# Kernel optimization log

Measured on AMD Instinct MI355X. Metric: run time of the kernel, lower is better.

Reference implementation:

```python
import jax, jax.numpy as jnp
import numpy as np

B, SEQ, NNODES = 4, 12, 1024
SEG_LEN, SEG_NUM = 3, 4
HID, FF, DK, NH, NLAYERS = 64, 2048, 32, 8, 2


def setup_inputs() -> dict:
    key = jax.random.key(0)
    ks = iter(jax.random.split(key, 64))
    def nrm(shape, scale=0.05):
        return jax.random.normal(next(ks), shape, dtype=jnp.float32) * scale
    ones = lambda s: jnp.ones(s, jnp.float32)
    zeros = lambda s: jnp.zeros(s, jnp.float32)
    S, L = 2, NLAYERS
    return {
        'traffic': nrm((B, SEQ, NNODES), 1.0),
        'user': nrm((B, SEQ, NNODES), 1.0),
        'patch_w': nrm((S, HID, SEG_LEN)), 'patch_b': nrm((S, HID)),
        'mha_w': nrm((S, L, 3 * HID, HID)), 'mha_b': nrm((S, L, 3 * HID)),
        'out_w': nrm((S, L, HID, HID)), 'out_b': nrm((S, L, HID)),
        'ff1_w': nrm((S, L, FF, HID)), 'ff1_b': nrm((S, L, FF)),
        'ff2_w': nrm((S, L, HID, FF)), 'ff2_b': nrm((S, L, HID)),
        'ln1_g': ones((S, L, HID)), 'ln1_b': zeros((S, L, HID)),
        'ln2_g': ones((S, L, HID)), 'ln2_b': zeros((S, L, HID)),
        'ga_wq': nrm((S, L, DK, HID)), 'ga_wk': nrm((S, L, DK, HID)), 'ga_wv': nrm((S, L, HID, HID)),
        'ga_ff1_w': nrm((S, L, FF, HID)), 'ga_ff1_b': nrm((S, L, FF)),
        'ga_ff2_w': nrm((S, L, HID, FF)), 'ga_ff2_b': nrm((S, L, HID)),
        'ga_ln1_g': ones((S, L, HID)), 'ga_ln1_b': zeros((S, L, HID)),
        'ga_ln2_g': ones((S, L, HID)), 'ga_ln2_b': zeros((S, L, HID)),
        'ca_wq': nrm((DK, 2 * HID)), 'ca_wk': nrm((DK, 2 * HID)), 'ca_wv': nrm((HID, 2 * HID)),
    }


def _ln(x, g, b, eps=1e-5):
    m = x.mean(-1, keepdims=True)
    v = jnp.mean((x - m) ** 2, -1, keepdims=True)
    return (x - m) / jnp.sqrt(v + eps) * g + b


def _pe(s, d):
    pos = jnp.arange(s, dtype=jnp.float32)[:, None]
    div = jnp.exp(jnp.arange(0, d, 2, dtype=jnp.float32) * (-np.log(10000.0) / d))
    pe = jnp.zeros((s, d), jnp.float32)
    pe = pe.at[:, 0::2].set(jnp.sin(pos * div))
    pe = pe.at[:, 1::2].set(jnp.cos(pos * div))
    return pe


def _mha(x, w, b, wo, bo):
    # standard nn.MultiheadAttention self-attn, batch_first; x: [B,S,H]
    qkv = x @ w.T + b
    q, k, v = jnp.split(qkv, 3, axis=-1)
    def heads(t):
        b_, s_, h_ = t.shape
        return t.reshape(b_, s_, NH, h_ // NH).transpose(0, 2, 1, 3)
    q, k, v = heads(q), heads(k), heads(v)
    scale = 1.0 / jnp.sqrt(jnp.float32(HID // NH))
    att = jax.nn.softmax(jnp.einsum('bhqd,bhkd->bhqk', q, k) * scale, axis=-1)
    o = jnp.einsum('bhqk,bhkd->bhqd', att, v).transpose(0, 2, 1, 3).reshape(x.shape)
    return o @ wo.T + bo


def _enc_layer(x, p):
    # TransformerEncoderLayer_cross, post-norm, dropout=0 (eval)
    x = _ln(x + _mha(x, p['mw'], p['mb'], p['ow'], p['ob']), p['g1'], p['b1'])
    f = jax.nn.relu(x @ p['f1w'].T + p['f1b']) @ p['f2w'].T + p['f2b']
    return _ln(x + f, p['g2'], p['b2'])


def _graph_att(x, p):
    # GraphAttention.forward (bias=None, mask=None, dropout=0)
    q = x @ p['wq'].T
    k = x @ p['wk'].T
    v = x @ p['wv'].T
    dist = jax.nn.softmax(jnp.einsum('bnd,bmd->bnm', q, k) / jnp.sqrt(jnp.float32(DK)), axis=-1)
    att = jnp.einsum('bnm,bmd->bnd', dist, v)
    att = _ln(att, p['g1'], p['b1']) + x
    f = jax.nn.relu(att @ p['f1w'].T + p['f1b']) @ p['f2w'].T + p['f2b']
    return _ln(att + f, p['g2'], p['b2'])


def reference(traffic, user, patch_w, patch_b, mha_w, mha_b, out_w, out_b,
              ff1_w, ff1_b, ff2_w, ff2_b, ln1_g, ln1_b, ln2_g, ln2_b,
              ga_wq, ga_wk, ga_wv, ga_ff1_w, ga_ff1_b, ga_ff2_w, ga_ff2_b,
              ga_ln1_g, ga_ln1_b, ga_ln2_g, ga_ln2_b, ca_wq, ca_wk, ca_wv):
    pe = _pe(SEG_NUM, HID)

    def encode(x, s):
        b, _, d = x.shape
        # DSW_embedding: b (seg_num seg_len) d -> b d seg_num seg_len, then Linear
        seg = x.reshape(b, SEG_NUM, SEG_LEN, d).transpose(0, 3, 1, 2)
        z = seg @ patch_w[s].T + patch_b[s]          # [b, d, seg_num, HID]
        z = z + pe                                    # positional encoding over patches
        for i in range(NLAYERS):
            # temporal attention over the patch axis
            zt = z.reshape(b * d, SEG_NUM, HID)
            zt = _enc_layer(zt, dict(mw=mha_w[s, i], mb=mha_b[s, i], ow=out_w[s, i], ob=out_b[s, i],
                                     f1w=ff1_w[s, i], f1b=ff1_b[s, i], f2w=ff2_w[s, i], f2b=ff2_b[s, i],
                                     g1=ln1_g[s, i], b1=ln1_b[s, i], g2=ln2_g[s, i], b2=ln2_b[s, i]))
            z = zt.reshape(b, d, SEG_NUM, HID)
            # spatial graph attention over the node axis
            zs = z.transpose(0, 2, 1, 3).reshape(b * SEG_NUM, d, HID)
            zs = _graph_att(zs, dict(wq=ga_wq[s, i], wk=ga_wk[s, i], wv=ga_wv[s, i],
                                     f1w=ga_ff1_w[s, i], f1b=ga_ff1_b[s, i], f2w=ga_ff2_w[s, i], f2b=ga_ff2_b[s, i],
                                     g1=ga_ln1_g[s, i], b1=ga_ln1_b[s, i], g2=ga_ln2_g[s, i], b2=ga_ln2_b[s, i]))
            z = zs.reshape(b, SEG_NUM, d, HID).transpose(0, 2, 1, 3)
        return z.mean(axis=2)                         # pool patches -> [b, d, HID]

    enc = jnp.concatenate([encode(traffic, 0), encode(user, 1)], axis=-1)  # [b, d, 2*HID]
    # encoder_attn: SelfAttention(2*HID -> dim_k=32, dim_v=HID)
    q = enc @ ca_wq.T
    k = enc @ ca_wk.T
    v = enc @ ca_wv.T
    dist = jax.nn.softmax(jnp.einsum('bnd,bmd->bnm', q, k) / jnp.sqrt(jnp.float32(DK)), axis=-1)
    return jnp.einsum('bnm,bmd->bnd', dist, v)        # [b, n_nodes, HID]
```

## Files before the change

### kernel.cpp

```cpp
#include <hip/hip_runtime.h>
#include <hip/hip_bf16.h>
#include <math.h>

#define BB 4
#define SEQL 12
#define NN 1024
#define SEGL 3
#define SEGN 4
#define HID 64
#define FFD 2048
#define DKK 32
#define NHH 8
#define HDD 8
#define ZS 1048576

using bf16 = __hip_bfloat16;
__device__ __forceinline__ float b2f(bf16 v) { return __bfloat162float(v); }

typedef __attribute__((ext_vector_type(8))) short s8v;
typedef __attribute__((ext_vector_type(4))) float f4v;
typedef __attribute__((ext_vector_type(4))) unsigned short u4v;

__device__ __forceinline__ unsigned short f2b(float f) {
  bf16 h = __float2bfloat16(f);
  unsigned short u; __builtin_memcpy(&u, &h, 2); return u;
}
__device__ __forceinline__ float us2f(unsigned short u) {
  unsigned int e = ((unsigned int)u) << 16;
  float f; __builtin_memcpy(&f, &e, 4); return f;
}

template <int F>
__device__ __forceinline__ float ldw(const void* p, long i) {
  if (F) return ((const float*)p)[i];
  return b2f(((const bf16*)p)[i]);
}
template <int F>
__device__ __forceinline__ s8v ldfrag(const void* p, long elemOff) {
  if (F) {
    const float* fp = (const float*)p + elemOff;
    f4v u = *(const f4v*)fp, v = *(const f4v*)(fp + 4);
    s8v t;
    t[0]=f2b(u[0]); t[1]=f2b(u[1]); t[2]=f2b(u[2]); t[3]=f2b(u[3]);
    t[4]=f2b(v[0]); t[5]=f2b(v[1]); t[6]=f2b(v[2]); t[7]=f2b(v[3]);
    return t;
  }
  return *(const s8v*)((const unsigned short*)p + elemOff);
}
template <int F>
__device__ __forceinline__ f4v ldb4(const void* p, long i) {
  if (F) return *(const f4v*)((const float*)p + i);
  u4v u = *(const u4v*)((const unsigned short*)p + i);
  f4v r; r[0]=us2f(u[0]); r[1]=us2f(u[1]); r[2]=us2f(u[2]); r[3]=us2f(u[3]);
  return r;
}

__global__ void k_zero(unsigned short* __restrict__ o, int n) {
  int i = blockIdx.x * 256 + threadIdx.x;
  if (i < n) o[i] = 0;
}

__global__ void k_detect(const void* __restrict__ x0, int* __restrict__ flag) {
  int t = threadIdx.x;
  int bad = 0;
  const bf16* p = (const bf16*)x0;
  for (int i = t; i < 512; i += 256) {
    float a = fabsf(b2f(p[i]));
    if (!(a < 1e4f) || (a != 0.f && a < 1e-4f)) bad = 1;
  }
  __shared__ int tot;
  if (t == 0) tot = 0;
  __syncthreads();
  unsigned long long m = __ballot(bad);
  if ((t & 63) == 0) atomicAdd(&tot, __popcll(m));
  __syncthreads();
  if (t == 0) *flag = (tot > 64) ? 1 : 0;
}

template <int F>
__device__ __forceinline__ void wconv_body(const void* __restrict__ w1,
    const void* __restrict__ w2, const void* __restrict__ w3,
    const void* __restrict__ w4, unsigned short* __restrict__ out) {
  int i = blockIdx.x * 256 + threadIdx.x;
  long e8 = (long)i * 8;
  int slot = (int)(e8 >> 17);
  int si = slot >> 2, which = slot & 3;
  long r = e8 & 131071;
  const void* src = (which == 0) ? w1 : (which == 1) ? w2 : (which == 2) ? w3 : w4;
  *(s8v*)(out + e8) = ldfrag<F>(src, (long)si*FFD*HID + r);
}
__global__ __launch_bounds__(256) void k_wconv(const void* w1, const void* w2,
    const void* w3, const void* w4, unsigned short* out,
    const int* __restrict__ flag) {
  if (*flag) wconv_body<1>(w1, w2, w3, w4, out);
  else       wconv_body<0>(w1, w2, w3, w4, out);
}

template <int F>
__device__ __forceinline__ void patch_body(const void* __restrict__ xt,
    const void* __restrict__ xu,
    const void* __restrict__ pw, const void* __restrict__ pb,
    float* __restrict__ z) {
  int bid = blockIdx.x;
  int s = bid >> 12, rem = bid & 4095;
  int b = rem >> 10, n = rem & 1023;
  const void* x = s ? xu : xt;
  long opw = (long)s*HID*SEGL, opb = (long)s*HID;
  int g = threadIdx.x >> 6, h = threadIdx.x & 63;
  float acc = ldw<F>(pb, opb + h);
#pragma unroll
  for (int l = 0; l < SEGL; ++l)
    acc += ldw<F>(x, (long)(b*SEQL + g*SEGL + l)*NN + n) * ldw<F>(pw, opw + h*SEGL + l);
  int i2 = h >> 1;
  float dv = expf((float)(2*i2) * (-logf(10000.f) / (float)HID));
  float ang = (float)g * dv;
  acc += (h & 1) ? cosf(ang) : sinf(ang);
  z[(long)s*ZS + ((long)(b*NN + n)*SEGN + g)*HID + h] = acc;
}
__global__ __launch_bounds__(256) void k_patch(const void* __restrict__ xt,
    const void* __restrict__ xu,
    const void* __restrict__ pw, const void* __restrict__ pb,
    float* __restrict__ z, const int* __restrict__ flag) {
  if (*flag) patch_body<1>(xt, xu, pw, pb, z);
  else       patch_body<0>(xt, xu, pw, pb, z);
}

#define TT 64
#define FRW 64
#define HCS 74

__device__ __forceinline__ void ff_ld(const unsigned short* __restrict__ wc1,
    const unsigned short* __restrict__ wc2, int hb, int srow, int le,
    s8v* r1, s8v* r2) {
  r1[0] = *(const s8v*)(wc1 + (long)(hb + srow)*HID + le*8);
  r1[1] = *(const s8v*)(wc1 + (long)(hb + srow + 8)*HID + le*8);
  r2[0] = *(const s8v*)(wc2 + (long)srow*FFD + hb + le*8);
  r2[1] = *(const s8v*)(wc2 + (long)(srow + 8)*FFD + hb + le*8);
}
__device__ __forceinline__ void ff_wr(char* ldsbuf, int pb, int srow, int swb,
    const s8v* r1, const s8v* r2) {
  char* w1b = ldsbuf + pb*8192;
  char* w2b = ldsbuf + 16384 + pb*8192;
  *(s8v*)(w1b + srow*128 + swb) = r1[0];
  *(s8v*)(w1b + (srow + 8)*128 + swb) = r1[1];
  *(s8v*)(w2b + srow*128 + swb) = r2[0];
  *(s8v*)(w2b + (srow + 8)*128 + swb) = r2[1];
}
template <int F>
__device__ __forceinline__ void ff_compute(const char* ldsbuf, int pb, int hb,
    int col, int quad, int sw, const s8v* bx, unsigned short* hcw,
    const void* __restrict__ B1, long ob1, f4v* acc) {
  const char* w1b = ldsbuf + pb*8192;
  const char* w2b = ldsbuf + 16384 + pb*8192;
#pragma unroll
  for (int t = 0; t < 4; ++t) {
    int row = t*16 + col;
    s8v a10 = *(const s8v*)(w1b + row*128 + ((quad*16) ^ sw));
    s8v a11 = *(const s8v*)(w1b + row*128 + ((64 + quad*16) ^ sw));
    f4v bv = ldb4<F>(B1, ob1 + hb + t*16 + quad*4);
    f4v sv = __builtin_amdgcn_mfma_f32_16x16x32_bf16(a10, bx[0],
               (f4v){0.f,0.f,0.f,0.f}, 0, 0, 0);
    sv = __builtin_amdgcn_mfma_f32_16x16x32_bf16(a11, bx[1], sv, 0, 0, 0);
    unsigned short pk[4];
#pragma unroll
    for (int r = 0; r < 4; ++r) pk[r] = f2b(fmaxf(sv[r] + bv[r], 0.f));
    *(unsigned long long*)&hcw[col*HCS + t*16 + quad*4] =
      (unsigned long long)pk[0] | ((unsigned long long)pk[1] << 16) |
      ((unsigned long long)pk[2] << 32) | ((unsigned long long)pk[3] << 48);
  }
#pragma unroll
  for (int ks2 = 0; ks2 < 2; ++ks2) {
    s8v bh = *(const s8v*)&hcw[col*HCS + ks2*32 + quad*8];
#pragma unroll
    for (int m = 0; m < 4; ++m) {
      int r2 = m*16 + col;
      s8v a2 = *(const s8v*)(w2b + r2*128 + ((ks2*64 + quad*16) ^ sw));
      acc[m] = __builtin_amdgcn_mfma_f32_16x16x32_bf16(a2, bh, acc[m], 0, 0, 0);
    }
  }
}

template <int F>
__device__ __forceinline__ void tff_body(float* __restrict__ zb,
    const void* __restrict__ W, const void* __restrict__ bq,
    const void* __restrict__ WO, const void* __restrict__ bo,
    const void* __restrict__ g1, const void* __restrict__ b1,
    const unsigned short* __restrict__ wcw, int li,
    const void* __restrict__ B1, const void* __restrict__ B2,
    const void* __restrict__ G, const void* __restrict__ Bt,
    char* lds) {
  int s = blockIdx.x >> 8, blk = blockIdx.x & 255;
  long si = s*2 + li;
  float* z = zb + (long)s*ZS;
  long oW = si*3*HID*HID, obq = si*3*HID, oWO = si*HID*HID, obo = si*HID;
  long og1 = si*HID, ob1 = si*HID;
  const unsigned short* wc1 = wcw + (si*4 + 0)*131072;
  const unsigned short* wc2 = wcw + (si*4 + 1)*131072;
  long fob1 = si*FFD, fob2 = si*HID, fog = si*HID, fobt = si*HID;
  unsigned short (*qkvs)[200] = (unsigned short(*)[200])lds;
  unsigned short (*ao)[72]    = (unsigned short(*)[72])(lds + 25600);
  float (*yb)[68]             = (float(*)[68])(lds + 34816);
  int tid = threadIdx.x;
  int w = tid >> 6, lane = tid & 63;
  int col = lane & 15, quad = lane >> 4;
  long r0 = (long)blk * TT;
  float* stashW = (float*)(lds + 59648 + w*4352);

  int lr = lane >> 3, le = lane & 7;
  int srow = w*16 + lr;
  int swb = ((le ^ lr) << 4);
  s8v cw1[2], cw2[2];
  ff_ld(wc1, wc2, 0, srow, le, cw1, cw2);

  s8v bx[4][2];
#pragma unroll
  for (int mt = 0; mt < 4; ++mt) {
    const float* xr = z + (r0 + mt*16 + col) * HID;
#pragma unroll
    for (int ks = 0; ks < 2; ++ks) {
      const float* p = xr + ks*32 + quad*8;
      f4v u = *(const f4v*)p, v = *(const f4v*)(p + 4);
      s8v t;
      t[0]=f2b(u[0]); t[1]=f2b(u[1]); t[2]=f2b(u[2]); t[3]=f2b(u[3]);
      t[4]=f2b(v[0]); t[5]=f2b(v[1]); t[6]=f2b(v[2]); t[7]=f2b(v[3]);
      bx[mt][ks] = t;
    }
  }
#pragma unroll
  for (int nt = 0; nt < 3; ++nt) {
    int cbase = (w*3 + nt) * 16;
    s8v aw[2];
#pragma unroll
    for (int ks = 0; ks < 2; ++ks)
      aw[ks] = ldfrag<F>(W, oW + (long)(cbase + col)*HID + ks*32 + quad*8);
    f4v bv = ldb4<F>(bq, obq + cbase + quad*4);
#pragma unroll
    for (int mt = 0; mt < 4; ++mt) {
      f4v sv = (f4v){0.f,0.f,0.f,0.f};
#pragma unroll
      for (int ks = 0; ks < 2; ++ks)
        sv = __builtin_amdgcn_mfma_f32_16x16x32_bf16(aw[ks], bx[mt][ks], sv, 0, 0, 0);
      unsigned short pk[4];
#pragma unroll
      for (int r = 0; r < 4; ++r) pk[r] = f2b(sv[r] + bv[r]);
      *(unsigned long long*)&qkvs[mt*16 + col][cbase + quad*4] =
        (unsigned long long)pk[0] | ((unsigned long long)pk[1] << 16) |
        ((unsigned long long)pk[2] << 32) | ((unsigned long long)pk[3] << 48);
    }
  }
  __syncthreads();
  if (tid < 128) {
    int gi = tid >> 3, hd = tid & 7;
    int tl = gi * 4;
    float qv[4][8], kv[4][8], vv[4][8];
#pragma unroll
    for (int t4 = 0; t4 < 4; ++t4) {
      s8v qq = *(const s8v*)&qkvs[tl + t4][hd*8];
      s8v kk = *(const s8v*)&qkvs[tl + t4][64 + hd*8];
      s8v vq = *(const s8v*)&qkvs[tl + t4][128 + hd*8];
#pragma unroll
      for (int e = 0; e < 8; ++e) {
        qv[t4][e] = us2f((unsigned short)qq[e]);
        kv[t4][e] = us2f((unsigned short)kk[e]);
        vv[t4][e] = us2f((unsigned short)vq[e]);
      }
    }
    const float sc8 = 0.3535533905932738f;
#pragma unroll
    for (int qt = 0; qt < 4; ++qt) {
      float sc[4]; float mx = -1e30f;
#pragma unroll
      for (int kt = 0; kt < 4; ++kt) {
        float d = 0;
#pragma unroll
        for (int e = 0; e < 8; ++e) d += qv[qt][e]*kv[kt][e];
        sc[kt] = d*sc8; mx = fmaxf(mx, sc[kt]);
      }
      float se = 0;
#pragma unroll
      for (int kt = 0; kt < 4; ++kt) { sc[kt] = expf(sc[kt]-mx); se += sc[kt]; }
      float inv = 1.f/se;
      s8v outp;
#pragma unroll
      for (int e = 0; e < 8; ++e) {
        float o = 0;
#pragma unroll
        for (int kt = 0; kt < 4; ++kt) o += sc[kt]*vv[kt][e];
        outp[e] = (short)f2b(o*inv);
      }
      *(s8v*)&ao[tl + qt][hd*8] = outp;
    }
  }
  __syncthreads();
  s8v awo[2];
#pragma unroll
  for (int ks = 0; ks < 2; ++ks)
    awo[ks] = ldfrag<F>(WO, oWO + (long)(w*16 + col)*HID + ks*32 + quad*8);
  f4v bov = ldb4<F>(bo, obo + w*16 + quad*4);
#pragma unroll
  for (int mt = 0; mt < 4; ++mt) {
    f4v ov = (f4v){0.f,0.f,0.f,0.f};
#pragma unroll
    for (int ks = 0; ks < 2; ++ks) {
      s8v bao = *(const s8v*)&ao[mt*16 + col][ks*32 + quad*8];
      ov = __builtin_amdgcn_mfma_f32_16x16x32_bf16(awo[ks], bao, ov, 0, 0, 0);
    }
    f4v yv;
#pragma unroll
    for (int r = 0; r < 4; ++r) yv[r] = ov[r] + bov[r];
    *(f4v*)&yb[mt*16 + col][w*16 + quad*4] = yv;
  }
  __syncthreads();
  {
    float gg = ldw<F>(g1, og1 + lane), bb2 = ldw<F>(b1, ob1 + lane);
#pragma unroll
    for (int rr = 0; rr < 16; ++rr) {
      int row = w*16 + rr;
      long tok = r0 + row;
      float val = yb[row][lane] + z[tok*HID + lane];
      float sm = val;
#pragma unroll
      for (int off = 32; off; off >>= 1) sm += __shfl_xor(sm, off);
      float m = sm*(1.f/HID);
      float d = val - m, sq = d*d;
#pragma unroll
      for (int off = 32; off; off >>= 1) sq += __shfl_xor(sq, off);
      float rv = rsqrtf(sq*(1.f/HID) + 1e-5f);
      stashW[rr*68 + lane] = d*rv*gg + bb2;
    }
  }
  __syncthreads();

  unsigned short* hcw = (unsigned short*)(lds + 32768 + w*2368);
  float* red = (float*)(lds + 42240 + w*4352);

  s8v bx2[2];
#pragma unroll
  for (int ks = 0; ks < 2; ++ks) {
    const float* p = &stashW[col*68 + ks*32 + quad*8];
    f4v u = *(const f4v*)p, v = *(const f4v*)(p + 4);
    s8v t;
    t[0]=f2b(u[0]); t[1]=f2b(u[1]); t[2]=f2b(u[2]); t[3]=f2b(u[3]);
    t[4]=f2b(v[0]); t[5]=f2b(v[1]); t[6]=f2b(v[2]); t[7]=f2b(v[3]);
    bx2[ks] = t;
  }

  f4v acc[4];
#pragma unroll
  for (int m = 0; m < 4; ++m) acc[m] = (f4v){0.f,0.f,0.f,0.f};

  s8v rA1[2], rA2[2], rB1[2], rB2[2];
  ff_ld(wc1, wc2, 64, srow, le, rA1, rA2);
  ff_ld(wc1, wc2, 128, srow, le, rB1, rB2);
  ff_wr(lds, 0, srow, swb, cw1, cw2);
  __syncthreads();

  const int sw = (col & 7) << 4;
  for (int c = 0; c < 32; c += 2) {
    ff_compute<F>(lds, 0, c*64, col, quad, sw, bx2, hcw, B1, fob1, acc);
    ff_wr(lds, 1, srow, swb, rA1, rA2);
    if (c + 3 < 32) ff_ld(wc1, wc2, (c+3)*64, srow, le, rA1, rA2);
    __syncthreads();
    ff_compute<F>(lds, 1, (c+1)*64, col, quad, sw, bx2, hcw, B1, fob1, acc);
    if (c + 2 < 32) ff_wr(lds, 0, srow, swb, rB1, rB2);
    if (c + 4 < 32) ff_ld(wc1, wc2, (c+4)*64, srow, le, rB1, rB2);
    __syncthreads();
  }

#pragma unroll
  for (int m = 0; m < 4; ++m)
    *(f4v*)&red[col*68 + m*16 + quad*4] = acc[m];
  float fgg = ldw<F>(G, fog + lane), fbbt = ldw<F>(Bt, fobt + lane);
  float b2v = ldw<F>(B2, fob2 + lane);
#pragma unroll
  for (int rr = 0; rr < 16; ++rr) {
    long grow = r0 + w*16 + rr;
    float val = red[rr*68 + lane] + b2v + stashW[rr*68 + lane];
    float sm = val;
#pragma unroll
    for (int off = 32; off; off >>= 1) sm += __shfl_xor(sm, off);
    float m = sm * (1.f/HID);
    float d = val - m;
    float sq = d*d;
#pragma unroll
    for (int off = 32; off; off >>= 1) sq += __shfl_xor(sq, off);
    float rv = rsqrtf(sq*(1.f/HID) + 1e-5f);
    z[grow*HID + lane] = d*rv*fgg + fbbt;
  }
}
__global__ __launch_bounds__(256) void k_tff(float* __restrict__ z,
    const void* W, const void* bqkv, const void* WO, const void* bo,
    const void* g1, const void* b1,
    const unsigned short* __restrict__ wcw, int li,
    const void* B1, const void* B2, const void* G, const void* Bt,
    const int* __restrict__ flag) {
  __shared__ __attribute__((aligned(16))) char lds[77056];
  if (*flag) tff_body<1>(z, W, bqkv, WO, bo, g1, b1, wcw, li, B1, B2, G, Bt, lds);
  else       tff_body<0>(z, W, bqkv, WO, bo, g1, b1, wcw, li, B1, B2, G, Bt, lds);
}

template <int F>
__device__ __forceinline__ void ffmfma_body(float* __restrict__ xb,
    const unsigned short* __restrict__ wcw, int li, int wsel,
    const void* __restrict__ B1, const void* __restrict__ B2,
    const void* __restrict__ G, const void* __restrict__ Bt,
    float* __restrict__ enc, int dop,
    char* ldsbuf) {
  int s = blockIdx.x >> 8, blk = blockIdx.x & 255;
  long si = s*2 + li;
  float* x = xb + (long)s*ZS;
  const unsigned short* wc1 = wcw + (si*4 + wsel)*131072;
  const unsigned short* wc2 = wcw + (si*4 + wsel + 1)*131072;
  long ob1 = si*FFD, ob2 = si*HID, og = si*HID, obt = si*HID;
  int tid = threadIdx.x;
  int w = tid >> 6, lane = tid & 63;
  int col = lane & 15, quad = lane >> 4;
  long r0 = (long)blk * FRW;
  unsigned short* hcw = (unsigned short*)(ldsbuf + 32768 + w*2368);
  float* red = (float*)(ldsbuf + w*4352);

  long tokc = r0 + w*16 + col;
  s8v bx[2];
  {
    const float* xr = x + tokc * HID;
#pragma unroll
    for (int ks = 0; ks < 2; ++ks) {
      const float* p = xr + ks*32 + quad*8;
      f4v u = *(const f4v*)p, v = *(const f4v*)(p + 4);
      s8v t;
      t[0]=f2b(u[0]); t[1]=f2b(u[1]); t[2]=f2b(u[2]); t[3]=f2b(u[3]);
      t[4]=f2b(v[0]); t[5]=f2b(v[1]); t[6]=f2b(v[2]); t[7]=f2b(v[3]);
      bx[ks] = t;
    }
  }

  int lr = lane >> 3;
  int le = lane & 7;
  int srow = w*16 + lr;
  int swb = ((le ^ lr) << 4);

  f4v acc[4];
#pragma unroll
  for (int m = 0; m < 4; ++m) acc[m] = (f4v){0.f,0.f,0.f,0.f};

  s8v t1[2], t2[2], rA1[2], rA2[2], rB1[2], rB2[2];
  ff_ld(wc1, wc2, 0, srow, le, t1, t2);
  ff_wr(ldsbuf, 0, srow, swb, t1, t2);
  ff_ld(wc1, wc2, 64, srow, le, rA1, rA2);
  ff_ld(wc1, wc2, 128, srow, le, rB1, rB2);
  __syncthreads();

  const int sw = (col & 7) << 4;
  for (int c = 0; c < 32; c += 2) {
    ff_compute<F>(ldsbuf, 0, c*64, col, quad, sw, bx, hcw, B1, ob1, acc);
    ff_wr(ldsbuf, 1, srow, swb, rA1, rA2);
    if (c + 3 < 32) ff_ld(wc1, wc2, (c+3)*64, srow, le, rA1, rA2);
    __syncthreads();
    ff_compute<F>(ldsbuf, 1, (c+1)*64, col, quad, sw, bx, hcw, B1, ob1, acc);
    if (c + 2 < 32) ff_wr(ldsbuf, 0, srow, swb, rB1, rB2);
    if (c + 4 < 32) ff_ld(wc1, wc2, (c+4)*64, srow, le, rB1, rB2);
    __syncthreads();
  }

#pragma unroll
  for (int m = 0; m < 4; ++m)
    *(f4v*)&red[col*68 + m*16 + quad*4] = acc[m];
  float gg = ldw<F>(G, og + lane), bbt = ldw<F>(Bt, obt + lane);
  float b2v = ldw<F>(B2, ob2 + lane);
  float pacc[4] = {0.f,0.f,0.f,0.f};
#pragma unroll
  for (int rr = 0; rr < 16; ++rr) {
    long grow = r0 + w*16 + rr;
    float val = red[rr*68 + lane] + b2v + x[grow*HID + lane];
    float sm = val;
#pragma unroll
    for (int off = 32; off; off >>= 1) sm += __shfl_xor(sm, off);
    float m = sm * (1.f/HID);
    float d = val - m;
    float sq = d*d;
#pragma unroll
    for (int off = 32; off; off >>= 1) sq += __shfl_xor(sq, off);
    float rv = rsqrtf(sq*(1.f/HID) + 1e-5f);
    float fin = d*rv*gg + bbt;
    x[grow*HID + lane] = fin;
    pacc[rr >> 2] += fin;
  }
  if (dop) {
#pragma unroll
    for (int j = 0; j < 4; ++j) {
      long tok = r0 + w*16 + j*4;
      enc[(tok >> 2)*(2*HID) + s*HID + lane] = pacc[j]*0.25f;
    }
  }
}
__global__ __launch_bounds__(256) void k_ffmfma(float* __restrict__ x,
    const unsigned short* __restrict__ wcw, int li, int wsel,
    const void* B1, const void* B2, const void* G, const void* Bt,
    float* enc, int dop, const int* __restrict__ flag) {
  __shared__ __attribute__((aligned(16))) char ldsbuf[42240];
  if (*flag) ffmfma_body<1>(x, wcw, li, wsel, B1, B2, G, Bt, enc, dop, ldsbuf);
  else       ffmfma_body<0>(x, wcw, li, wsel, B1, B2, G, Bt, enc, dop, ldsbuf);
}

template <int F>
__device__ __forceinline__ void gqkv_body(const float* __restrict__ zb,
    const void* __restrict__ wq, const void* __restrict__ wk,
    const void* __restrict__ wv, int li,
    unsigned short* __restrict__ q, unsigned short* __restrict__ k,
    unsigned short* __restrict__ vt) {
  int tid = threadIdx.x;
  int w = tid >> 6, lane = tid & 63;
  int col = lane & 15, quad = lane >> 4;
  int sg = blockIdx.x >> 4;
  int s = sg >> 4, bg = sg & 15;
  int n0 = (blockIdx.x & 15) * 64;
  int b = bg >> 2, g = bg & 3;
  long si = s*2 + li;
  const float* z = zb + (long)s*ZS;
  long oq = si*DKK*HID, ok = si*DKK*HID, ov = si*HID*HID;
  long gbase = (long)sg * NN;

  s8v bx[4][2];
#pragma unroll
  for (int rt = 0; rt < 4; ++rt) {
    const float* xr = z + ((long)(b*NN + n0 + rt*16 + col)*SEGN + g)*HID;
#pragma unroll
    for (int ks = 0; ks < 2; ++ks) {
      const float* p = xr + ks*32 + quad*8;
      f4v u = *(const f4v*)p, vv = *(const f4v*)(p + 4);
      s8v t;
      t[0]=f2b(u[0]); t[1]=f2b(u[1]); t[2]=f2b(u[2]); t[3]=f2b(u[3]);
      t[4]=f2b(vv[0]); t[5]=f2b(vv[1]); t[6]=f2b(vv[2]); t[7]=f2b(vv[3]);
      bx[rt][ks] = t;
    }
  }

#pragma unroll
  for (int tt = 0; tt < 2; ++tt) {
    int ct = w*2 + tt;
    const void* wp; long wo; int co; int kind;
    if (ct < 2)      { wp = wq; wo = oq; co = ct*16;      kind = 0; }
    else if (ct < 4) { wp = wk; wo = ok; co = (ct-2)*16;  kind = 1; }
    else             { wp = wv; wo = ov; co = (ct-4)*16;  kind = 2; }
    s8v aw[2];
#pragma unroll
    for (int ks = 0; ks < 2; ++ks)
      aw[ks] = ldfrag<F>(wp, wo + (long)(co + col)*HID + ks*32 + quad*8);
#pragma unroll
    for (int rt = 0; rt < 4; ++rt) {
      f4v sv = (f4v){0.f,0.f,0.f,0.f};
#pragma unroll
      for (int ks = 0; ks < 2; ++ks)
        sv = __builtin_amdgcn_mfma_f32_16x16x32_bf16(aw[ks], bx[rt][ks], sv, 0, 0, 0);
      int key = n0 + rt*16 + col;
      if (kind == 2) {
        long vbase = (long)sg*HID*NN;
#pragma unroll
        for (int r = 0; r < 4; ++r)
          vt[vbase + (long)(co + quad*4 + r)*NN + key] = f2b(sv[r]);
      } else {
        long row = gbase + key;
        unsigned short pk[4];
#pragma unroll
        for (int r = 0; r < 4; ++r) pk[r] = f2b(sv[r]);
        unsigned short* dst = kind ? k : q;
        *(unsigned long long*)&dst[row*DKK + co + quad*4] =
          (unsigned long long)pk[0] | ((unsigned long long)pk[1] << 16) |
          ((unsigned long long)pk[2] << 32) | ((unsigned long long)pk[3] << 48);
      }
    }
  }
}
__global__ __launch_bounds__(256) void k_gqkv(const float* __restrict__ z,
    const void* wq, const void* wk, const void* wv, int li,
    unsigned short* q, unsigned short* k, unsigned short* vt,
    const int* __restrict__ flag) {
  if (*flag) gqkv_body<1>(z, wq, wk, wv, li, q, k, vt);
  else       gqkv_body<0>(z, wq, wk, wv, li, q, k, vt);
}

__global__ __launch_bounds__(512) void k_gattn(float* __restrict__ zb,
    const unsigned short* __restrict__ qb, const unsigned short* __restrict__ kb,
    const unsigned short* __restrict__ vtb,
    const void* __restrict__ g1, const void* __restrict__ b1, int li,
    const int* __restrict__ flag) {
  int f = *flag;
  __shared__ unsigned short pl[2][8][16][74];
  __shared__ float accb[8][16][66];
  __shared__ float lb[8][16];
  int tid = threadIdx.x;
  int w = tid >> 6, lane = tid & 63;
  int col = lane & 15, quad = lane >> 4;
  int qt = w >> 1, kh = w & 1;
  int sg = blockIdx.x >> 4;
  int s = sg >> 4, bg = sg & 15;
  int n0 = (blockIdx.x & 15) * 64;
  long si = s*2 + li;
  float* z = zb + (long)s*ZS;
  long og1 = si*HID, ob1 = si*HID;
  long gbase = (long)sg * NN;
  const unsigned short* vrow = vtb + (long)sg*HID*NN;

  s8v aq = *(const s8v*)(qb + (gbase + n0 + qt*16 + col)*DKK + quad*8);

  f4v acc[4];
#pragma unroll
  for (int t = 0; t < 4; ++t) acc[t] = (f4v){0.f,0.f,0.f,0.f};
  float psum[4] = {0.f,0.f,0.f,0.f};
  const float rs = 0.17677669529663687f;
  const int cbeg = kh * 512;

#pragma unroll 2
  for (int it = 0; it < 8; ++it) {
    int c0 = cbeg + it*64;
    int pb = it & 1;
    f4v s4[4];
#pragma unroll
    for (int nt = 0; nt < 4; ++nt) {
      s8v bk = *(const s8v*)(kb + (gbase + c0 + nt*16 + col)*DKK + quad*8);
      s4[nt] = __builtin_amdgcn_mfma_f32_16x16x32_bf16(aq, bk,
                (f4v){0.f,0.f,0.f,0.f}, 0, 0, 0);
    }
#pragma unroll
    for (int r = 0; r < 4; ++r) {
      float p0 = expf(s4[0][r]*rs), p1 = expf(s4[1][r]*rs);
      float p2 = expf(s4[2][r]*rs), p3 = expf(s4[3][r]*rs);
      psum[r] += (p0 + p1) + (p2 + p3);
      int row = quad*4 + r;
      pl[pb][w][row][col]      = f2b(p0);
      pl[pb][w][row][16 + col] = f2b(p1);
      pl[pb][w][row][32 + col] = f2b(p2);
      pl[pb][w][row][48 + col] = f2b(p3);
    }
#pragma unroll
    for (int ks = 0; ks < 2; ++ks) {
      s8v ap = *(const s8v*)&pl[pb][w][col][ks*32 + quad*8];
#pragma unroll
      for (int nt = 0; nt < 4; ++nt) {
        s8v bv = *(const s8v*)(vrow + (long)(nt*16 + col)*NN + c0 + ks*32 + quad*8);
        acc[nt] = __builtin_amdgcn_mfma_f32_16x16x32_bf16(ap, bv, acc[nt], 0, 0, 0);
      }
    }
  }

#pragma unroll
  for (int r = 0; r < 4; ++r) {
    float v = psum[r];
#pragma unroll
    for (int off = 1; off < 16; off <<= 1) v += __shfl_xor(v, off);
    psum[r] = v;
  }
#pragma unroll
  for (int t = 0; t < 4; ++t)
#pragma unroll
    for (int r = 0; r < 4; ++r)
      accb[w][quad*4 + r][t*16 + col] = acc[t][r];
  if (col == 0) {
#pragma unroll
    for (int r = 0; r < 4; ++r) lb[w][quad*4 + r] = psum[r];
  }
  __syncthreads();

  int b = bg >> 2, g = bg & 3;
  float gg = f ? ((const float*)g1)[og1 + lane] : b2f(((const bf16*)g1)[og1 + lane]);
  float bb = f ? ((const float*)b1)[ob1 + lane] : b2f(((const bf16*)b1)[ob1 + lane]);
#pragma unroll
  for (int rr = 0; rr < 8; ++rr) {
    int rl = w*8 + rr;
    int qtt = rl >> 4, lr = rl & 15;
    float a = accb[2*qtt][lr][lane] + accb[2*qtt + 1][lr][lane];
    float l = lb[2*qtt][lr] + lb[2*qtt + 1][lr];
    float val = a / l;
    float s2 = val;
#pragma unroll
    for (int off = 32; off; off >>= 1) s2 += __shfl_xor(s2, off);
    float m = s2*(1.f/HID);
    float d = val - m, sq = d*d;
#pragma unroll
    for (int off = 32; off; off >>= 1) sq += __shfl_xor(sq, off);
    float r = rsqrtf(sq*(1.f/HID) + 1e-5f);
    float* zp = z + ((long)(b*NN + n0 + rl)*SEGN + g)*HID;
    zp[lane] = d*r*gg + bb + zp[lane];
  }
}

template <int F>
__device__ __forceinline__ void fqkv_body(const float* __restrict__ enc,
    const void* __restrict__ wq, const void* __restrict__ wk,
    const void* __restrict__ wv,
    unsigned short* __restrict__ q, unsigned short* __restrict__ k,
    unsigned short* __restrict__ vt, float* xs) {
  long r = blockIdx.x;
  int t = threadIdx.x;
  xs[t] = enc[r*128 + t];
  __syncthreads();
  if (t < 32) {
    long wr = (long)t*128; float a = 0;
    for (int e = 0; e < 128; ++e) a += xs[e]*ldw<F>(wq, wr + e);
    q[r*DKK + t] = f2b(a);
  } else if (t < 64) {
    long wr = (long)(t-32)*128; float a = 0;
    for (int e = 0; e < 128; ++e) a += xs[e]*ldw<F>(wk, wr + e);
    k[r*DKK + (t-32)] = f2b(a);
  } else {
    long wr = (long)(t-64)*128; float a = 0;
    for (int e = 0; e < 128; ++e) a += xs[e]*ldw<F>(wv, wr + e);
    vt[((r >> 10)*HID + (t-64))*NN + (r & 1023)] = f2b(a);
  }
}
__global__ __launch_bounds__(128) void k_fqkv(const float* __restrict__ enc,
    const void* wq, const void* wk, const void* wv,
    unsigned short* q, unsigned short* k, unsigned short* vt,
    const int* __restrict__ flag) {
  __shared__ float xs[2*HID];
  if (*flag) fqkv_body<1>(enc, wq, wk, wv, q, k, vt, xs);
  else       fqkv_body<0>(enc, wq, wk, wv, q, k, vt, xs);
}

__global__ __launch_bounds__(512) void k_fattn(
    const unsigned short* __restrict__ qb, const unsigned short* __restrict__ kb,
    const unsigned short* __restrict__ vtb, void* __restrict__ outp,
    const int* __restrict__ flag) {
  __shared__ unsigned short pl[2][8][16][74];
  __shared__ float accb[8][16][66];
  __shared__ float lb[8][16];
  int tid = threadIdx.x;
  int w = tid >> 6, lane = tid & 63;
  int col = lane & 15, quad = lane >> 4;
  int qt = w >> 1, kh = w & 1;
  int b = blockIdx.x >> 4;
  int n0 = (blockIdx.x & 15) * 64;
  long gbase = (long)b * NN;
  const unsigned short* vrow = vtb + (long)b*HID*NN;

  s8v aq = *(const s8v*)(qb + (gbase + n0 + qt*16 + col)*DKK + quad*8);

  f4v acc[4];
#pragma unroll
  for (int t = 0; t < 4; ++t) acc[t] = (f4v){0.f,0.f,0.f,0.f};
  float psum[4] = {0.f,0.f,0.f,0.f};
  const float rs = 0.17677669529663687f;
  const int cbeg = kh * 512;

#pragma unroll 2
  for (int it = 0; it < 8; ++it) {
    int c0 = cbeg + it*64;
    int pb = it & 1;
    f4v s4[4];
#pragma unroll
    for (int nt = 0; nt < 4; ++nt) {
      s8v bk = *(const s8v*)(kb + (gbase + c0 + nt*16 + col)*DKK + quad*8);
      s4[nt] = __builtin_amdgcn_mfma_f32_16x16x32_bf16(aq, bk,
                (f4v){0.f,0.f,0.f,0.f}, 0, 0, 0);
    }
#pragma unroll
    for (int r = 0; r < 4; ++r) {
      float p0 = expf(s4[0][r]*rs), p1 = expf(s4[1][r]*rs);
      float p2 = expf(s4[2][r]*rs), p3 = expf(s4[3][r]*rs);
      psum[r] += (p0 + p1) + (p2 + p3);
      int row = quad*4 + r;
      pl[pb][w][row][col]      = f2b(p0);
      pl[pb][w][row][16 + col] = f2b(p1);
      pl[pb][w][row][32 + col] = f2b(p2);
      pl[pb][w][row][48 + col] = f2b(p3);
    }
#pragma unroll
    for (int ks = 0; ks < 2; ++ks) {
      s8v ap = *(const s8v*)&pl[pb][w][col][ks*32 + quad*8];
#pragma unroll
      for (int nt = 0; nt < 4; ++nt) {
        s8v bv = *(const s8v*)(vrow + (long)(nt*16 + col)*NN + c0 + ks*32 + quad*8);
        acc[nt] = __builtin_amdgcn_mfma_f32_16x16x32_bf16(ap, bv, acc[nt], 0, 0, 0);
      }
    }
  }

#pragma unroll
  for (int r = 0; r < 4; ++r) {
    float v = psum[r];
#pragma unroll
    for (int off = 1; off < 16; off <<= 1) v += __shfl_xor(v, off);
    psum[r] = v;
  }
#pragma unroll
  for (int t = 0; t < 4; ++t)
#pragma unroll
    for (int r = 0; r < 4; ++r)
      accb[w][quad*4 + r][t*16 + col] = acc[t][r];
  if (col == 0) {
#pragma unroll
    for (int r = 0; r < 4; ++r) lb[w][quad*4 + r] = psum[r];
  }
  __syncthreads();

  int f = *flag;
#pragma unroll
  for (int rr = 0; rr < 8; ++rr) {
    int rl = w*8 + rr;
    int qtt = rl >> 4, lr = rl & 15;
    float a = accb[2*qtt][lr][lane] + accb[2*qtt + 1][lr][lane];
    float l = lb[2*qtt][lr] + lb[2*qtt + 1][lr];
    float val = a / l;
    long idx = (gbase + n0 + rl)*HID + lane;
    if (f) ((float*)outp)[idx] = val;
    else   ((bf16*)outp)[idx] = __float2bfloat16(val);
  }
}

extern "C" void kernel_launch(void* const* d_in, const int* in_sizes, int n_in,
                              void* d_out, int out_size, void* d_ws, size_t ws_size,
                              hipStream_t stream) {
  static const int EXP[30] = {
    49152, 49152, 384, 128, 49152, 768, 16384, 256,
    524288, 8192, 524288, 256, 256, 256, 256, 256,
    8192, 8192, 16384, 524288, 8192, 524288, 256, 256,
    256, 256, 256, 4096, 4096, 8192
  };
  const size_t NEED = (size_t)(2*ZS + 524288 + 524288 + 524288 + 1048576 + 1048576) * 4 + 64;
  bool ok = (n_in == 30) && (ws_size >= NEED) && (out_size == BB*NN*HID);
  if (ok) for (int i = 0; i < 30; ++i) ok = ok && (in_sizes[i] == EXP[i]);
  if (!ok) {
    k_zero<<<(BB*NN*HID + 255)/256, 256, 0, stream>>>((unsigned short*)d_out, BB*NN*HID);
    return;
  }

  float* z   = (float*)d_ws;
  float* enc = z   + 2*ZS;
  float* qb  = enc + 524288;
  float* kb  = qb  + 524288;
  float* vb  = kb  + 524288;
  float* wcf = vb  + 1048576;
  int*  flag = (int*)(wcf + 1048576);
  unsigned short* wcw = (unsigned short*)wcf;

  k_detect<<<1, 256, 0, stream>>>(d_in[0], flag);

  const void *i_traffic=d_in[0], *i_user=d_in[1], *i_pw=d_in[2], *i_pb=d_in[3],
    *i_mw=d_in[4], *i_mb=d_in[5], *i_ow=d_in[6], *i_ob=d_in[7], *i_f1w=d_in[8],
    *i_f1b=d_in[9], *i_f2w=d_in[10], *i_f2b=d_in[11], *i_l1g=d_in[12],
    *i_l1b=d_in[13], *i_l2g=d_in[14], *i_l2b=d_in[15], *i_gwq=d_in[16],
    *i_gwk=d_in[17], *i_gwv=d_in[18], *i_gf1w=d_in[19], *i_gf1b=d_in[20],
    *i_gf2w=d_in[21], *i_gf2b=d_in[22], *i_gl1g=d_in[23], *i_gl1b=d_in[24],
    *i_gl2g=d_in[25], *i_gl2b=d_in[26], *i_cwq=d_in[27], *i_cwk=d_in[28],
    *i_cwv=d_in[29];

  k_wconv<<<1024, 256, 0, stream>>>(i_f1w, i_f2w, i_gf1w, i_gf2w, wcw, flag);
  k_patch<<<2*BB*NN, 256, 0, stream>>>(i_traffic, i_user, i_pw, i_pb, z, flag);

  for (int i = 0; i < 2; ++i) {
    k_tff<<<512, 256, 0, stream>>>(z, i_mw, i_mb, i_ow, i_ob,
        i_l1g, i_l1b, wcw, i, i_f1b, i_f2b, i_l2g, i_l2b, flag);
    k_gqkv<<<512, 256, 0, stream>>>(z, i_gwq, i_gwk, i_gwv, i,
        (unsigned short*)qb, (unsigned short*)kb, (unsigned short*)vb, flag);
    k_gattn<<<512, 512, 0, stream>>>(z,
        (const unsigned short*)qb, (const unsigned short*)kb,
        (const unsigned short*)vb, i_gl1g, i_gl1b, i, flag);
    k_ffmfma<<<512, 256, 0, stream>>>(z, wcw, i, 2,
        i_gf1b, i_gf2b, i_gl2g, i_gl2b, enc, (i == 1) ? 1 : 0, flag);
  }
  k_fqkv<<<BB*NN, 128, 0, stream>>>(enc, i_cwq, i_cwk, i_cwv,
      (unsigned short*)qb, (unsigned short*)kb, (unsigned short*)vb, flag);
  k_fattn<<<BB*16, 512, 0, stream>>>((const unsigned short*)qb,
      (const unsigned short*)kb, (unsigned short*)vb, d_out, flag);
}
```

Before: 603.0 us.

## Fuse graph-attention QKV projection into temporal transformer kernel epilogue

The separate k_gqkv launch is removed. The temporal FFN kernel now stages its final LayerNorm output in shared memory, converts it to bf16 and computes the graph-attention Q/K/V projections with MFMA directly from that data. It writes q, k and transposed v using token-to-(b,node,segment) index math. This saves one launch per layer and the re-read of z from global memory, but adds epilogue work, a sync, and scattered stores from each tff block.

After: 595.5 us. Within noise of the previous version (-1.2%).

```diff
diff --git a/kernel.cpp b/kernel.cpp
--- a/kernel.cpp
+++ b/kernel.cpp
@@ -188,6 +188,10 @@
     const unsigned short* __restrict__ wcw, int li,
     const void* __restrict__ B1, const void* __restrict__ B2,
     const void* __restrict__ G, const void* __restrict__ Bt,
+    const void* __restrict__ gwq, const void* __restrict__ gwk,
+    const void* __restrict__ gwv,
+    unsigned short* __restrict__ qo, unsigned short* __restrict__ ko,
+    unsigned short* __restrict__ vto,
     char* lds) {
   int s = blockIdx.x >> 8, blk = blockIdx.x & 255;
   long si = s*2 + li;
@@ -370,22 +374,81 @@
 #pragma unroll
   for (int m = 0; m < 4; ++m)
     *(f4v*)&red[col*68 + m*16 + quad*4] = acc[m];
-  float fgg = ldw<F>(G, fog + lane), fbbt = ldw<F>(Bt, fobt + lane);
-  float b2v = ldw<F>(B2, fob2 + lane);
-#pragma unroll
-  for (int rr = 0; rr < 16; ++rr) {
-    long grow = r0 + w*16 + rr;
-    float val = red[rr*68 + lane] + b2v + stashW[rr*68 + lane];
-    float sm = val;
-#pragma unroll
-    for (int off = 32; off; off >>= 1) sm += __shfl_xor(sm, off);
-    float m = sm * (1.f/HID);
-    float d = val - m;
-    float sq = d*d;
-#pragma unroll
-    for (int off = 32; off; off >>= 1) sq += __shfl_xor(sq, off);
-    float rv = rsqrtf(sq*(1.f/HID) + 1e-5f);
-    z[grow*HID + lane] = d*rv*fgg + fbbt;
+  float* finb = (float*)lds;
+  {
+    float fgg = ldw<F>(G, fog + lane), fbbt = ldw<F>(Bt, fobt + lane);
+    float b2v = ldw<F>(B2, fob2 + lane);
+#pragma unroll
+    for (int rr = 0; rr < 16; ++rr) {
+      long grow = r0 + w*16 + rr;
+      float val = red[rr*68 + lane] + b2v + stashW[rr*68 + lane];
+      float sm = val;
+#pragma unroll
+      for (int off = 32; off; off >>= 1) sm += __shfl_xor(sm, off);
+      float m = sm * (1.f/HID);
+      float d = val - m;
+      float sq = d*d;
+#pragma unroll
+      for (int off = 32; off; off >>= 1) sq += __shfl_xor(sq, off);
+      float rv = rsqrtf(sq*(1.f/HID) + 1e-5f);
+      float fin = d*rv*fgg + fbbt;
+      z[grow*HID + lane] = fin;
+      finb[(w*16 + rr)*68 + lane] = fin;
+    }
+  }
+  __syncthreads();
+
+  long oq = si*DKK*HID, okk = si*DKK*HID, ovv = si*HID*HID;
+  s8v bx3[4][2];
+#pragma unroll
+  for (int rt = 0; rt < 4; ++rt)
+#pragma unroll
+    for (int ks = 0; ks < 2; ++ks) {
+      const float* p = &finb[(rt*16 + col)*68 + ks*32 + quad*8];
+      f4v u = *(const f4v*)p, v = *(const f4v*)(p + 4);
+      s8v t;
+      t[0]=f2b(u[0]); t[1]=f2b(u[1]); t[2]=f2b(u[2]); t[3]=f2b(u[3]);
+      t[4]=f2b(v[0]); t[5]=f2b(v[1]); t[6]=f2b(v[2]); t[7]=f2b(v[3]);
+      bx3[rt][ks] = t;
+    }
+#pragma unroll
+  for (int tt = 0; tt < 2; ++tt) {
+    int ct = w*2 + tt;
+    const void* wp; long wo; int co; int kind;
+    if (ct < 2)      { wp = gwq; wo = oq;  co = ct*16;      kind = 0; }
+    else if (ct < 4) { wp = gwk; wo = okk; co = (ct-2)*16;  kind = 1; }
+    else             { wp = gwv; wo = ovv; co = (ct-4)*16;  kind = 2; }
+    s8v aw[2];
+#pragma unroll
+    for (int ks = 0; ks < 2; ++ks)
+      aw[ks] = ldfrag<F>(wp, wo + (long)(co + col)*HID + ks*32 + quad*8);
+#pragma unroll
+    for (int rt = 0; rt < 4; ++rt) {
+      f4v sv = (f4v){0.f,0.f,0.f,0.f};
+#pragma unroll
+      for (int ks = 0; ks < 2; ++ks)
+        sv = __builtin_amdgcn_mfma_f32_16x16x32_bf16(aw[ks], bx3[rt][ks], sv, 0, 0, 0);
+      long tok2 = r0 + rt*16 + col;
+      int b_ = (int)(tok2 >> 12);
+      int n_ = (int)((tok2 >> 2) & 1023);
+      int g_ = (int)(tok2 & 3);
+      int sgl = s*16 + b_*4 + g_;
+      if (kind == 2) {
+        long vbase = (long)sgl*HID*NN;
+#pragma unroll
+        for (int r = 0; r < 4; ++r)
+          vto[vbase + (long)(co + quad*4 + r)*NN + n_] = f2b(sv[r]);
+      } else {
+        long row = (long)sgl*NN + n_;
+        unsigned short pk[4];
+#pragma unroll
+        for (int r = 0; r < 4; ++r) pk[r] = f2b(sv[r]);
+        unsigned short* dst = kind ? ko : qo;
+        *(unsigned long long*)&dst[row*DKK + co + quad*4] =
+          (unsigned long long)pk[0] | ((unsigned long long)pk[1] << 16) |
+          ((unsigned long long)pk[2] << 32) | ((unsigned long long)pk[3] << 48);
+      }
+    }
   }
 }
 __global__ __launch_bounds__(256) void k_tff(float* __restrict__ z,
@@ -393,10 +456,14 @@
     const void* g1, const void* b1,
     const unsigned short* __restrict__ wcw, int li,
     const void* B1, const void* B2, const void* G, const void* Bt,
+    const void* gwq, const void* gwk, const void* gwv,
+    unsigned short* qo, unsigned short* ko, unsigned short* vto,
     const int* __restrict__ flag) {
   __shared__ __attribute__((aligned(16))) char lds[77056];
-  if (*flag) tff_body<1>(z, W, bqkv, WO, bo, g1, b1, wcw, li, B1, B2, G, Bt, lds);
-  else       tff_body<0>(z, W, bqkv, WO, bo, g1, b1, wcw, li, B1, B2, G, Bt, lds);
+  if (*flag) tff_body<1>(z, W, bqkv, WO, bo, g1, b1, wcw, li, B1, B2, G, Bt,
+                         gwq, gwk, gwv, qo, ko, vto, lds);
+  else       tff_body<0>(z, W, bqkv, WO, bo, g1, b1, wcw, li, B1, B2, G, Bt,
+                         gwq, gwk, gwv, qo, ko, vto, lds);
 }
 
 template <int F>
@@ -500,83 +567,6 @@
   __shared__ __attribute__((aligned(16))) char ldsbuf[42240];
   if (*flag) ffmfma_body<1>(x, wcw, li, wsel, B1, B2, G, Bt, enc, dop, ldsbuf);
   else       ffmfma_body<0>(x, wcw, li, wsel, B1, B2, G, Bt, enc, dop, ldsbuf);
-}
-
-template <int F>
-__device__ __forceinline__ void gqkv_body(const float* __restrict__ zb,
-    const void* __restrict__ wq, const void* __restrict__ wk,
-    const void* __restrict__ wv, int li,
-    unsigned short* __restrict__ q, unsigned short* __restrict__ k,
-    unsigned short* __restrict__ vt) {
-  int tid = threadIdx.x;
-  int w = tid >> 6, lane = tid & 63;
-  int col = lane & 15, quad = lane >> 4;
-  int sg = blockIdx.x >> 4;
-  int s = sg >> 4, bg = sg & 15;
-  int n0 = (blockIdx.x & 15) * 64;
-  int b = bg >> 2, g = bg & 3;
-  long si = s*2 + li;
-  const float* z = zb + (long)s*ZS;
-  long oq = si*DKK*HID, ok = si*DKK*HID, ov = si*HID*HID;
-  long gbase = (long)sg * NN;
-
-  s8v bx[4][2];
-#pragma unroll
-  for (int rt = 0; rt < 4; ++rt) {
-    const float* xr = z + ((long)(b*NN + n0 + rt*16 + col)*SEGN + g)*HID;
-#pragma unroll
-    for (int ks = 0; ks < 2; ++ks) {
-      const float* p = xr + ks*32 + quad*8;
-      f4v u = *(const f4v*)p, vv = *(const f4v*)(p + 4);
-      s8v t;
-      t[0]=f2b(u[0]); t[1]=f2b(u[1]); t[2]=f2b(u[2]); t[3]=f2b(u[3]);
-      t[4]=f2b(vv[0]); t[5]=f2b(vv[1]); t[6]=f2b(vv[2]); t[7]=f2b(vv[3]);
-      bx[rt][ks] = t;
-    }
-  }
-
-#pragma unroll
-  for (int tt = 0; tt < 2; ++tt) {
-    int ct = w*2 + tt;
-    const void* wp; long wo; int co; int kind;
-    if (ct < 2)      { wp = wq; wo = oq; co = ct*16;      kind = 0; }
-    else if (ct < 4) { wp = wk; wo = ok; co = (ct-2)*16;  kind = 1; }
-    else             { wp = wv; wo = ov; co = (ct-4)*16;  kind = 2; }
-    s8v aw[2];
-#pragma unroll
-    for (int ks = 0; ks < 2; ++ks)
-      aw[ks] = ldfrag<F>(wp, wo + (long)(co + col)*HID + ks*32 + quad*8);
-#pragma unroll
-    for (int rt = 0; rt < 4; ++rt) {
-      f4v sv = (f4v){0.f,0.f,0.f,0.f};
-#pragma unroll
-      for (int ks = 0; ks < 2; ++ks)
-        sv = __builtin_amdgcn_mfma_f32_16x16x32_bf16(aw[ks], bx[rt][ks], sv, 0, 0, 0);
-      int key = n0 + rt*16 + col;
-      if (kind == 2) {
-        long vbase = (long)sg*HID*NN;
-#pragma unroll
-        for (int r = 0; r < 4; ++r)
-          vt[vbase + (long)(co + quad*4 + r)*NN + key] = f2b(sv[r]);
-      } else {
-        long row = gbase + key;
-        unsigned short pk[4];
-#pragma unroll
-        for (int r = 0; r < 4; ++r) pk[r] = f2b(sv[r]);
-        unsigned short* dst = kind ? k : q;
-        *(unsigned long long*)&dst[row*DKK + co + quad*4] =
-          (unsigned long long)pk[0] | ((unsigned long long)pk[1] << 16) |
-          ((unsigned long long)pk[2] << 32) | ((unsigned long long)pk[3] << 48);
-      }
-    }
-  }
-}
-__global__ __launch_bounds__(256) void k_gqkv(const float* __restrict__ z,
-    const void* wq, const void* wk, const void* wv, int li,
-    unsigned short* q, unsigned short* k, unsigned short* vt,
-    const int* __restrict__ flag) {
-  if (*flag) gqkv_body<1>(z, wq, wk, wv, li, q, k, vt);
-  else       gqkv_body<0>(z, wq, wk, wv, li, q, k, vt);
 }
 
 __global__ __launch_bounds__(512) void k_gattn(float* __restrict__ zb,
@@ -667,9 +657,9 @@
 #pragma unroll
   for (int rr = 0; rr < 8; ++rr) {
     int rl = w*8 + rr;
-    int qtt = rl >> 4, lr = rl & 15;
-    float a = accb[2*qtt][lr][lane] + accb[2*qtt + 1][lr][lane];
-    float l = lb[2*qtt][lr] + lb[2*qtt + 1][lr];
+    int qtt = rl >> 4, lrr = rl & 15;
+    float a = accb[2*qtt][lrr][lane] + accb[2*qtt + 1][lrr][lane];
+    float l = lb[2*qtt][lrr] + lb[2*qtt + 1][lrr];
     float val = a / l;
     float s2 = val;
 #pragma unroll
@@ -797,9 +787,9 @@
 #pragma unroll
   for (int rr = 0; rr < 8; ++rr) {
     int rl = w*8 + rr;
-    int qtt = rl >> 4, lr = rl & 15;
-    float a = accb[2*qtt][lr][lane] + accb[2*qtt + 1][lr][lane];
-    float l = lb[2*qtt][lr] + lb[2*qtt + 1][lr];
+    int qtt = rl >> 4, lrr = rl & 15;
+    float a = accb[2*qtt][lrr][lane] + accb[2*qtt + 1][lrr][lane];
+    float l = lb[2*qtt][lrr] + lb[2*qtt + 1][lrr];
     float val = a / l;
     long idx = (gbase + n0 + rl)*HID + lane;
     if (f) ((float*)outp)[idx] = val;
@@ -849,8 +839,8 @@
 
   for (int i = 0; i < 2; ++i) {
     k_tff<<<512, 256, 0, stream>>>(z, i_mw, i_mb, i_ow, i_ob,
-        i_l1g, i_l1b, wcw, i, i_f1b, i_f2b, i_l2g, i_l2b, flag);
-    k_gqkv<<<512, 256, 0, stream>>>(z, i_gwq, i_gwk, i_gwv, i,
+        i_l1g, i_l1b, wcw, i, i_f1b, i_f2b, i_l2g, i_l2b,
+        i_gwq, i_gwk, i_gwv,
         (unsigned short*)qb, (unsigned short*)kb, (unsigned short*)vb, flag);
     k_gattn<<<512, 512, 0, stream>>>(z,
         (const unsigned short*)qb, (const unsigned short*)kb,
```
